# Kernel optimization log

Hardware: AMD Instinct MI355X
Metric: run time of the kernel (lower is better)

Reference implementation:

```python
import jax, jax.numpy as jnp
import numpy as np


def setup_inputs() -> dict:
    key = jax.random.key(0)
    ks = jax.random.split(key, 6)
    B, S, AD, QD, A = 64, 2048, 1024, 1024, 1024
    scale = 0.02
    return {
        "input": jax.random.normal(ks[0], (B, QD), dtype=jnp.float32),
        "context": jax.random.normal(ks[1], (B, S, AD), dtype=jnp.float32),
        "W_pre": jax.random.normal(ks[2], (A, AD), dtype=jnp.float32) * scale,
        "b_pre": jax.random.normal(ks[3], (A,), dtype=jnp.float32) * scale,
        "W_q": jax.random.normal(ks[4], (A, QD), dtype=jnp.float32) * scale,
        "v": jax.random.normal(ks[5], (A,), dtype=jnp.float32) * scale,
    }


def reference(input, context, W_pre, b_pre, W_q, v):
    # precompute = linear_pre(context): [B, S, A]
    precompute = jnp.einsum("bsd,ad->bsa", context, W_pre) + b_pre
    # targetT = linear_q(input): [B, A], broadcast over sourceL
    targetT = jnp.einsum("bq,aq->ba", input, W_q)
    tmp = jnp.tanh(precompute + targetT[:, None, :])  # [B, S, A]
    energy = jnp.einsum("bsa,a->bs", tmp, v)          # linear_v, [B, S]
    score = jax.nn.softmax(energy, axis=1)             # softmax over sourceL
    weightedContext = jnp.einsum("bs,bsd->bd", score, context)
    return weightedContext, score, precompute
```

## Files before the change

### kernel.cpp

```cpp
#include <hip/hip_runtime.h>
#include <hip/hip_bf16.h>

#define BB   64
#define SS   2048
#define MM   (BB*SS)
#define NN   1024
#define KK   1024

typedef short bf16x8s __attribute__((ext_vector_type(8)));
typedef float f32x4   __attribute__((ext_vector_type(4)));

__device__ __forceinline__ short f2bf(float f) {
    union { __hip_bfloat16 h; short s; } u;
    u.h = __float2bfloat16(f);
    return u.s;
}

__device__ __forceinline__ bf16x8s cvt8(float4 a, float4 b) {
    bf16x8s r;
    r[0] = f2bf(a.x); r[1] = f2bf(a.y); r[2] = f2bf(a.z); r[3] = f2bf(a.w);
    r[4] = f2bf(b.x); r[5] = f2bf(b.y); r[6] = f2bf(b.z); r[7] = f2bf(b.w);
    return r;
}

__device__ __forceinline__ float tanh_fast(float x) {
    x = fminf(8.0f, fmaxf(-8.0f, x));
    float e = __expf(2.0f * x);
    return (e - 1.0f) / (e + 1.0f);
}

__device__ __forceinline__ void load_lds16(const void* g, void* l) {
    __builtin_amdgcn_global_load_lds(
        (const __attribute__((address_space(1))) unsigned int*)g,
        (__attribute__((address_space(3))) unsigned int*)l,
        16, 0, 0);
}

__global__ void cvt_bf16_kernel(const float* __restrict__ src,
                                __hip_bfloat16* __restrict__ dst, int n8) {
    int i = blockIdx.x * blockDim.x + threadIdx.x;
    const int stride = gridDim.x * blockDim.x;
    const float4* s4 = (const float4*)src;
    bf16x8s* d8 = (bf16x8s*)dst;
    for (; i < n8; i += stride) {
        d8[i] = cvt8(s4[i * 2], s4[i * 2 + 1]);
    }
}

__global__ void targetT_kernel(const float* __restrict__ input,
                               const float* __restrict__ W_q,
                               float* __restrict__ tgt) {
    __shared__ float inp[KK];
    const int t = threadIdx.x;
    const int b = blockIdx.x;
    const float* inRow = input + (size_t)b * KK;
    for (int i = t; i < KK; i += 256) inp[i] = inRow[i];
    __syncthreads();
    const int w = t >> 6, lane = t & 63;
    const int nbase = blockIdx.y * 256 + w * 64;
    for (int i = 0; i < 64; i++) {
        const int n = nbase + i;
        const float* wq = W_q + (size_t)n * KK;
        float a = 0.f;
        #pragma unroll
        for (int j = 0; j < 16; j++) a += wq[lane + 64 * j] * inp[lane + 64 * j];
        #pragma unroll
        for (int o = 32; o; o >>= 1) a += __shfl_xor(a, o);
        if (lane == 0) tgt[(size_t)b * NN + n] = a;
    }
}

__global__ __launch_bounds__(512, 2) void gemm8_kernel(
    const __hip_bfloat16* __restrict__ ctxb,
    const __hip_bfloat16* __restrict__ wpb,
    const float* __restrict__ bpre,
    const float* __restrict__ tgt,
    const float* __restrict__ vvec,
    float* __restrict__ pre,
    float* __restrict__ energy4,
    int row0)
{
    __shared__ __align__(16) char lds[131072];

    const int nwg  = gridDim.x;
    const int orig = blockIdx.x;
    const int swz  = (orig & 7) * (nwg >> 3) + (orig >> 3);
    const int mTile = swz >> 2;
    const int nTile = swz & 3;
    const int blockM = mTile * 256;
    const int blockN = nTile * 256;

    const int t = threadIdx.x, w = t >> 6, lane = t & 63;
    const int wm = w >> 2, wn = w & 3;
    const int l15 = lane & 15;

    const int r0  = t >> 3;
    const int lc0 = ((t & 7) * 16) ^ ((r0 & 7) << 4);
    const char* aSrc = (const char*)ctxb + (size_t)(blockM + r0) * 2048 + lc0;
    const char* bSrc = (const char*)wpb  + (size_t)(blockN + r0) * 2048 + lc0;

#define STAGE_A(buf, half, T) do { \
    load_lds16(aSrc + (half)*262144 +          (T)*128, &lds[(buf)*32768 + (half)*16384 +        w*1024]); \
    load_lds16(aSrc + (half)*262144 + 131072 + (T)*128, &lds[(buf)*32768 + (half)*16384 + 8192 + w*1024]); \
} while(0)
#define STAGE_B(buf, half, T) do { \
    load_lds16(bSrc + (half)*262144 +          (T)*128, &lds[65536 + (buf)*32768 + (half)*16384 +        w*1024]); \
    load_lds16(bSrc + (half)*262144 + 131072 + (T)*128, &lds[65536 + (buf)*32768 + (half)*16384 + 8192 + w*1024]); \
} while(0)

    const int c16 = (lane >> 4) * 16;
    const int xo  = (lane & 7) << 4;
    const int bk0 = c16 ^ xo;
    const int bk1 = (64 + c16) ^ xo;
    const int aBase = wm * 16384 + l15 * 128;
    const int bBase = 65536 + wn * 8192 + l15 * 128;

    bf16x8s curA[4][2], B0f[2][2], B1f[2][2];

#define READ_A(buf, mbase) do { \
    _Pragma("unroll") \
    for (int mf = 0; mf < 4; mf++) { \
        curA[mf][0] = *(const bf16x8s*)&lds[(buf)*32768 + aBase + ((mbase)+mf)*2048 + bk0]; \
        curA[mf][1] = *(const bf16x8s*)&lds[(buf)*32768 + aBase + ((mbase)+mf)*2048 + bk1]; \
    } } while(0)
#define READ_B(dst, buf, nbase) do { \
    _Pragma("unroll") \
    for (int nf = 0; nf < 2; nf++) { \
        dst[nf][0] = *(const bf16x8s*)&lds[(buf)*32768 + bBase + ((nbase)+nf)*2048 + bk0]; \
        dst[nf][1] = *(const bf16x8s*)&lds[(buf)*32768 + bBase + ((nbase)+nf)*2048 + bk1]; \
    } } while(0)

    f32x4 acc[8][4];
    #pragma unroll
    for (int m = 0; m < 8; m++)
        #pragma unroll
        for (int n = 0; n < 4; n++)
            acc[m][n] = f32x4{0.f, 0.f, 0.f, 0.f};

#define MFMA_Q(mbase, B, nbase) do { \
    __builtin_amdgcn_s_setprio(1); \
    _Pragma("unroll") \
    for (int ks = 0; ks < 2; ks++) \
        _Pragma("unroll") \
        for (int mf = 0; mf < 4; mf++) \
            _Pragma("unroll") \
            for (int nf = 0; nf < 2; nf++) \
                acc[(mbase)+mf][(nbase)+nf] = __builtin_amdgcn_mfma_f32_16x16x32_bf16( \
                    curA[mf][ks], B[nf][ks], acc[(mbase)+mf][(nbase)+nf], 0, 0, 0); \
    __builtin_amdgcn_s_setprio(0); \
} while(0)

#define PH_MID() do { __builtin_amdgcn_sched_barrier(0); \
    __builtin_amdgcn_s_barrier(); \
    asm volatile("s_waitcnt lgkmcnt(0)"); \
    __builtin_amdgcn_sched_barrier(0); } while(0)
#define PH_END() do { __builtin_amdgcn_sched_barrier(0); \
    __builtin_amdgcn_s_barrier(); } while(0)
#define VMCNT(n) do { asm volatile("s_waitcnt vmcnt(" #n ")"); \
    __builtin_amdgcn_sched_barrier(0); } while(0)

    STAGE_A(0, 0, 0); STAGE_A(0, 1, 0);
    STAGE_B(0, 0, 0); STAGE_B(0, 1, 0);
    STAGE_B(1, 0, 1); STAGE_B(1, 1, 1);
    VMCNT(4);
    __builtin_amdgcn_s_barrier();

    #pragma unroll 1
    for (int i = 0; i < 7; i++) {
        const int Tn1 = 2 * i + 1, Tn2 = 2 * i + 2, Tn3 = 2 * i + 3;
        READ_A(0, 0); READ_B(B0f, 0, 0);
        STAGE_A(1, 0, Tn1);
        PH_MID(); MFMA_Q(0, B0f, 0); PH_END();
        READ_B(B1f, 0, 2);
        STAGE_A(1, 1, Tn1);
        PH_MID(); MFMA_Q(0, B1f, 2); PH_END();
        READ_A(0, 4);
        STAGE_B(0, 0, Tn2);
        PH_MID(); MFMA_Q(4, B0f, 0); PH_END();
        STAGE_B(0, 1, Tn2);
        PH_MID(); MFMA_Q(4, B1f, 2);
        VMCNT(4);
        PH_END();
        READ_A(1, 0); READ_B(B0f, 1, 0);
        STAGE_A(0, 0, Tn2);
        PH_MID(); MFMA_Q(0, B0f, 0); PH_END();
        READ_B(B1f, 1, 2);
        STAGE_A(0, 1, Tn2);
        PH_MID(); MFMA_Q(0, B1f, 2); PH_END();
        READ_A(1, 4);
        STAGE_B(1, 0, Tn3);
        PH_MID(); MFMA_Q(4, B0f, 0); PH_END();
        STAGE_B(1, 1, Tn3);
        PH_MID(); MFMA_Q(4, B1f, 2);
        VMCNT(4);
        PH_END();
    }

    READ_A(0, 0); READ_B(B0f, 0, 0);
    STAGE_A(1, 0, 15);
    PH_MID(); MFMA_Q(0, B0f, 0); PH_END();
    READ_B(B1f, 0, 2);
    STAGE_A(1, 1, 15);
    PH_MID(); MFMA_Q(0, B1f, 2); PH_END();
    READ_A(0, 4);
    PH_MID(); MFMA_Q(4, B0f, 0); PH_END();
    PH_MID(); MFMA_Q(4, B1f, 2);
    VMCNT(0);
    PH_END();
    READ_A(1, 0); READ_B(B0f, 1, 0);
    PH_MID(); MFMA_Q(0, B0f, 0); PH_END();
    READ_B(B1f, 1, 2);
    PH_MID(); MFMA_Q(0, B1f, 2); PH_END();
    READ_A(1, 4);
    PH_MID(); MFMA_Q(4, B0f, 0); PH_END();
    PH_MID(); MFMA_Q(4, B1f, 2);

    const int bIdx = (row0 + blockM) >> 11;
    float bp[4], tq[4], vv[4];
    #pragma unroll
    for (int nf = 0; nf < 4; nf++) {
        const int col = blockN + wn * 64 + nf * 16 + l15;
        bp[nf] = bpre[col];
        tq[nf] = tgt[(size_t)bIdx * NN + col];
        vv[nf] = vvec[col];
    }
    const int gr0 = blockM + wm * 128 + ((lane >> 4) << 2);
    const int colBase = blockN + wn * 64 + l15;
    float* epart = energy4 + (size_t)nTile * MM;

    #pragma unroll
    for (int mf = 0; mf < 8; mf++) {
        #pragma unroll
        for (int j = 0; j < 4; j++) {
            const size_t rg = (size_t)row0 + gr0 + mf * 16 + j;
            float* prow = pre + rg * NN + colBase;
            float e = 0.f;
            #pragma unroll
            for (int nf = 0; nf < 4; nf++) {
                const float p = acc[mf][nf][j] + bp[nf];
                prow[nf * 16] = p;
                e += tanh_fast(p + tq[nf]) * vv[nf];
            }
            e += __shfl_xor(e, 1);
            e += __shfl_xor(e, 2);
            e += __shfl_xor(e, 4);
            e += __shfl_xor(e, 8);
            if (l15 == 0) epart[rg] = e;
        }
    }
#undef STAGE_A
#undef STAGE_B
#undef READ_A
#undef READ_B
#undef MFMA_Q
#undef PH_MID
#undef PH_END
#undef VMCNT
}

__global__ __launch_bounds__(256, 2) void gemm_energy_kernel(
    const float* __restrict__ ctx, const float* __restrict__ wpre,
    const float* __restrict__ bpre, const float* __restrict__ tgt,
    const float* __restrict__ vvec, float* __restrict__ pre,
    float* __restrict__ energy4)
{
    __shared__ __align__(16) float As[128 * 32];
    __shared__ __align__(16) float Bs[128 * 32];

    const int orig = blockIdx.x;
    const int swz  = (orig & 7) * 1024 + (orig >> 3);
    const int mTile = swz >> 3;
    const int nTile = swz & 7;
    const size_t blockM = (size_t)mTile * 128;
    const int    blockN = nTile * 128;

    const int t = threadIdx.x, w = t >> 6, lane = t & 63;

    size_t aoff[4], boff[4];
    #pragma unroll
    for (int i = 0; i < 4; i++) {
        const int bb    = i * 4096 + w * 1024 + lane * 16;
        const int row   = bb >> 7;
        const int physc = bb & 127;
        const int logc  = physc ^ ((row & 7) << 4);
        aoff[i] = (blockM + (size_t)row) * (KK * 4) + logc;
        boff[i] = ((size_t)(blockN + row)) * (KK * 4) + logc;
    }
    const char* ctxB  = (const char*)ctx;
    const char* wpreB = (const char*)wpre;

    const int wm = (w >> 1) * 64, wn = (w & 1) * 64;

    int fa0[4], fa1[4], fb0[4], fb1[4];
    const int c0 = (lane >> 4) * 32;
    #pragma unroll
    for (int m = 0; m < 4; m++) {
        const int rA = wm + m * 16 + (lane & 15);
        const int sA = (rA & 7) << 4;
        fa0[m] = rA * 128 + (c0 ^ sA);
        fa1[m] = rA * 128 + ((c0 + 16) ^ sA);
        const int rB = wn + m * 16 + (lane & 15);
        const int sB = (rB & 7) << 4;
        fb0[m] = rB * 128 + (c0 ^ sB);
        fb1[m] = rB * 128 + ((c0 + 16) ^ sB);
    }

    f32x4 acc[4][4];
    #pragma unroll
    for (int m = 0; m < 4; m++)
        #pragma unroll
        for (int n = 0; n < 4; n++)
            acc[m][n] = f32x4{0.f, 0.f, 0.f, 0.f};

    for (int kt = 0; kt < KK / 32; kt++) {
        __syncthreads();
        #pragma unroll
        for (int i = 0; i < 4; i++) {
            load_lds16(ctxB  + aoff[i] + (size_t)kt * 128,
                       (char*)As + i * 4096 + w * 1024);
            load_lds16(wpreB + boff[i] + (size_t)kt * 128,
                       (char*)Bs + i * 4096 + w * 1024);
        }
        __syncthreads();

        bf16x8s af[4], bfr[4];
        #pragma unroll
        for (int m = 0; m < 4; m++) {
            float4 x0 = *(const float4*)((const char*)As + fa0[m]);
            float4 x1 = *(const float4*)((const char*)As + fa1[m]);
            af[m] = cvt8(x0, x1);
            float4 y0 = *(const float4*)((const char*)Bs + fb0[m]);
            float4 y1 = *(const float4*)((const char*)Bs + fb1[m]);
            bfr[m] = cvt8(y0, y1);
        }
        #pragma unroll
        for (int m = 0; m < 4; m++)
            #pragma unroll
            for (int n = 0; n < 4; n++)
                acc[m][n] = __builtin_amdgcn_mfma_f32_16x16x32_bf16(
                    af[m], bfr[n], acc[m][n], 0, 0, 0);
    }

    const int bIdx = (int)(blockM >> 11);
    float bp[4], tq[4], vv[4];
    #pragma unroll
    for (int n = 0; n < 4; n++) {
        const int col = blockN + wn + n * 16 + (lane & 15);
        bp[n] = bpre[col];
        tq[n] = tgt[(size_t)bIdx * NN + col];
        vv[n] = vvec[col];
    }
    const int colBase = blockN + wn + (lane & 15);

    #pragma unroll
    for (int m = 0; m < 4; m++) {
        const size_t rbase = blockM + wm + m * 16 + ((lane >> 4) << 2);
        #pragma unroll
        for (int j = 0; j < 4; j++) {
            const size_t rg = rbase + j;
            float* prow = pre + rg * NN + colBase;
            float e = 0.f;
            #pragma unroll
            for (int n = 0; n < 4; n++) {
                const float p = acc[m][n][j] + bp[n];
                prow[n * 16] = p;
                e += tanh_fast(p + tq[n]) * vv[n];
            }
            e += __shfl_xor(e, 1);
            e += __shfl_xor(e, 2);
            e += __shfl_xor(e, 4);
            e += __shfl_xor(e, 8);
            if ((lane & 15) == 0) atomicAdd(&energy4[rg], e);
        }
    }
}

__global__ void softmax_kernel(const float* __restrict__ energy4,
                               float* __restrict__ score) {
    const int b = blockIdx.x, t = threadIdx.x;
    const int w = t >> 6, lane = t & 63;
    const size_t base = (size_t)b * SS;
    float x[8] = {0.f, 0.f, 0.f, 0.f, 0.f, 0.f, 0.f, 0.f};
    #pragma unroll
    for (int p = 0; p < 4; p++) {
        const float4* e4 = (const float4*)(energy4 + (size_t)p * MM + base);
        float4 v0 = e4[t * 2], v1 = e4[t * 2 + 1];
        x[0] += v0.x; x[1] += v0.y; x[2] += v0.z; x[3] += v0.w;
        x[4] += v1.x; x[5] += v1.y; x[6] += v1.z; x[7] += v1.w;
    }

    float mx = x[0];
    #pragma unroll
    for (int i = 1; i < 8; i++) mx = fmaxf(mx, x[i]);
    #pragma unroll
    for (int o = 32; o; o >>= 1) mx = fmaxf(mx, __shfl_xor(mx, o));
    __shared__ float rmax[4], rsum[4];
    if (lane == 0) rmax[w] = mx;
    __syncthreads();
    mx = fmaxf(fmaxf(rmax[0], rmax[1]), fmaxf(rmax[2], rmax[3]));

    float s = 0.f;
    #pragma unroll
    for (int i = 0; i < 8; i++) { x[i] = __expf(x[i] - mx); s += x[i]; }
    #pragma unroll
    for (int o = 32; o; o >>= 1) s += __shfl_xor(s, o);
    if (lane == 0) rsum[w] = s;
    __syncthreads();
    s = rsum[0] + rsum[1] + rsum[2] + rsum[3];
    const float inv = 1.0f / s;

    float* sc = score + base + t * 8;
    #pragma unroll
    for (int i = 0; i < 8; i++) sc[i] = x[i] * inv;
}

__global__ void wctx_bf16_kernel(const __hip_bfloat16* __restrict__ ctxb,
                                 const float* __restrict__ score,
                                 float* __restrict__ wc) {
    const int b = blockIdx.x, scnk = blockIdx.y, t = threadIdx.x;
    __shared__ float ss[256];
    ss[t] = score[(size_t)b * SS + scnk * 256 + t];
    __syncthreads();
    const ushort4* cr = (const ushort4*)(ctxb + ((size_t)b * SS + (size_t)scnk * 256) * KK) + t;
    float4 a = {0.f, 0.f, 0.f, 0.f};
    #pragma unroll 4
    for (int s = 0; s < 256; s++) {
        const ushort4 c = cr[(size_t)s * 256];
        const float wgt = ss[s];
        a.x += wgt * __uint_as_float((unsigned)c.x << 16);
        a.y += wgt * __uint_as_float((unsigned)c.y << 16);
        a.z += wgt * __uint_as_float((unsigned)c.z << 16);
        a.w += wgt * __uint_as_float((unsigned)c.w << 16);
    }
    float* o = wc + (size_t)b * KK + t * 4;
    atomicAdd(o + 0, a.x);
    atomicAdd(o + 1, a.y);
    atomicAdd(o + 2, a.z);
    atomicAdd(o + 3, a.w);
}

__global__ void wctx_kernel(const float* __restrict__ ctx,
                            const float* __restrict__ score,
                            float* __restrict__ wc) {
    const int b = blockIdx.x, scnk = blockIdx.y, t = threadIdx.x;
    __shared__ float ss[256];
    ss[t] = score[(size_t)b * SS + scnk * 256 + t];
    __syncthreads();
    const float4* cr = (const float4*)(ctx + ((size_t)b * SS + (size_t)scnk * 256) * KK) + t;
    float4 a = {0.f, 0.f, 0.f, 0.f};
    #pragma unroll 4
    for (int s = 0; s < 256; s++) {
        const float4 c = cr[(size_t)s * 256];
        const float wgt = ss[s];
        a.x += wgt * c.x; a.y += wgt * c.y; a.z += wgt * c.z; a.w += wgt * c.w;
    }
    float* o = wc + (size_t)b * KK + t * 4;
    atomicAdd(o + 0, a.x);
    atomicAdd(o + 1, a.y);
    atomicAdd(o + 2, a.z);
    atomicAdd(o + 3, a.w);
}

extern "C" void kernel_launch(void* const* d_in, const int* in_sizes, int n_in,
                              void* d_out, int out_size, void* d_ws, size_t ws_size,
                              hipStream_t stream) {
    const float* input = (const float*)d_in[0];
    const float* ctx   = (const float*)d_in[1];
    const float* W_pre = (const float*)d_in[2];
    const float* b_pre = (const float*)d_in[3];
    const float* W_q   = (const float*)d_in[4];
    const float* v     = (const float*)d_in[5];

    float* out   = (float*)d_out;
    float* wc    = out;
    float* score = out + 65536;
    float* pre   = out + 65536 + 131072;

    float* tgt     = (float*)d_ws;
    float* energy4 = (float*)((char*)d_ws + 262144);
    __hip_bfloat16* wpb  = (__hip_bfloat16*)((char*)d_ws + 262144 + 2097152);
    __hip_bfloat16* ctxb = (__hip_bfloat16*)((char*)d_ws + 262144 + 2097152 + 2097152);

    long long avail = (long long)ws_size - 262144LL - 2097152LL - 2097152LL;
    long long cr = avail > 0 ? (avail / (KK * 2)) : 0;
    cr &= ~511LL;
    int chunk_rows = (int)(cr > MM ? MM : cr);

    hipMemsetAsync(wc, 0, (size_t)BB * KK * sizeof(float), stream);

    targetT_kernel<<<dim3(BB, 4), 256, 0, stream>>>(input, W_q, tgt);

    if (chunk_rows >= 512) {
        cvt_bf16_kernel<<<512, 256, 0, stream>>>(W_pre, wpb, NN * KK / 8);
        for (int r0 = 0; r0 < MM; r0 += chunk_rows) {
            const int rows = (MM - r0) < chunk_rows ? (MM - r0) : chunk_rows;
            const int n8 = rows * KK / 8;
            const int cgrid = (n8 + 255) / 256 > 4096 ? 4096 : (n8 + 255) / 256;
            cvt_bf16_kernel<<<cgrid, 256, 0, stream>>>(
                ctx + (size_t)r0 * KK, ctxb, n8);
            gemm8_kernel<<<dim3((rows / 256) * 4), 512, 0, stream>>>(
                ctxb, wpb, b_pre, tgt, v, pre, energy4, r0);
        }
    } else {
        hipMemsetAsync(energy4, 0, (size_t)4 * MM * sizeof(float), stream);
        gemm_energy_kernel<<<dim3((MM / 128) * (NN / 128)), 256, 0, stream>>>(
            ctx, W_pre, b_pre, tgt, v, pre, energy4);
    }

    softmax_kernel<<<dim3(BB), 256, 0, stream>>>(energy4, score);

    if (chunk_rows >= MM) {
        wctx_bf16_kernel<<<dim3(BB, 8), 256, 0, stream>>>(ctxb, score, wc);
    } else {
        wctx_kernel<<<dim3(BB, 8), 256, 0, stream>>>(ctx, score, wc);
    }
}
```

Before: 620.3 us.

## Halve GEMM pipeline phases per K-tile and use rcp-based tanh

Restructures the bf16 GEMM main loop from eight quarter-phases per double-buffer iteration to four half-phases. Each phase now issues all four B fragments and 32 MFMAs, stages full A/B tiles in one macro, and drops the explicit lgkmcnt(0) waits. This cuts barrier count and gives the scheduler larger MFMA blocks. It also rewrites tanh_fast using a hardware reciprocal instead of a division. The cost is more live B registers and looser control over when LDS reads complete; with the explicit lgkmcnt waits gone, completion of those reads is left to the compiler.

```diff
diff --git a/kernel.cpp b/kernel.cpp
--- a/kernel.cpp
+++ b/kernel.cpp
@@ -26,7 +26,7 @@
 __device__ __forceinline__ float tanh_fast(float x) {
     x = fminf(8.0f, fmaxf(-8.0f, x));
     float e = __expf(2.0f * x);
-    return (e - 1.0f) / (e + 1.0f);
+    return 1.0f - 2.0f * __builtin_amdgcn_rcpf(e + 1.0f);
 }
 
 __device__ __forceinline__ void load_lds16(const void* g, void* l) {
@@ -99,13 +99,17 @@
     const char* aSrc = (const char*)ctxb + (size_t)(blockM + r0) * 2048 + lc0;
     const char* bSrc = (const char*)wpb  + (size_t)(blockN + r0) * 2048 + lc0;
 
-#define STAGE_A(buf, half, T) do { \
-    load_lds16(aSrc + (half)*262144 +          (T)*128, &lds[(buf)*32768 + (half)*16384 +        w*1024]); \
-    load_lds16(aSrc + (half)*262144 + 131072 + (T)*128, &lds[(buf)*32768 + (half)*16384 + 8192 + w*1024]); \
+#define STAGE_AF(buf, T) do { \
+    load_lds16(aSrc +          (T)*128, &lds[(buf)*32768 +         w*1024]); \
+    load_lds16(aSrc + 131072 + (T)*128, &lds[(buf)*32768 +  8192 + w*1024]); \
+    load_lds16(aSrc + 262144 + (T)*128, &lds[(buf)*32768 + 16384 + w*1024]); \
+    load_lds16(aSrc + 393216 + (T)*128, &lds[(buf)*32768 + 24576 + w*1024]); \
 } while(0)
-#define STAGE_B(buf, half, T) do { \
-    load_lds16(bSrc + (half)*262144 +          (T)*128, &lds[65536 + (buf)*32768 + (half)*16384 +        w*1024]); \
-    load_lds16(bSrc + (half)*262144 + 131072 + (T)*128, &lds[65536 + (buf)*32768 + (half)*16384 + 8192 + w*1024]); \
+#define STAGE_BF(buf, T) do { \
+    load_lds16(bSrc +          (T)*128, &lds[65536 + (buf)*32768 +         w*1024]); \
+    load_lds16(bSrc + 131072 + (T)*128, &lds[65536 + (buf)*32768 +  8192 + w*1024]); \
+    load_lds16(bSrc + 262144 + (T)*128, &lds[65536 + (buf)*32768 + 16384 + w*1024]); \
+    load_lds16(bSrc + 393216 + (T)*128, &lds[65536 + (buf)*32768 + 24576 + w*1024]); \
 } while(0)
 
     const int c16 = (lane >> 4) * 16;
@@ -115,7 +119,7 @@
     const int aBase = wm * 16384 + l15 * 128;
     const int bBase = 65536 + wn * 8192 + l15 * 128;
 
-    bf16x8s curA[4][2], B0f[2][2], B1f[2][2];
+    bf16x8s curA[4][2], Bf[4][2];
 
 #define READ_A(buf, mbase) do { \
     _Pragma("unroll") \
@@ -123,11 +127,11 @@
         curA[mf][0] = *(const bf16x8s*)&lds[(buf)*32768 + aBase + ((mbase)+mf)*2048 + bk0]; \
         curA[mf][1] = *(const bf16x8s*)&lds[(buf)*32768 + aBase + ((mbase)+mf)*2048 + bk1]; \
     } } while(0)
-#define READ_B(dst, buf, nbase) do { \
+#define READ_B(buf) do { \
     _Pragma("unroll") \
-    for (int nf = 0; nf < 2; nf++) { \
-        dst[nf][0] = *(const bf16x8s*)&lds[(buf)*32768 + bBase + ((nbase)+nf)*2048 + bk0]; \
-        dst[nf][1] = *(const bf16x8s*)&lds[(buf)*32768 + bBase + ((nbase)+nf)*2048 + bk1]; \
+    for (int nf = 0; nf < 4; nf++) { \
+        Bf[nf][0] = *(const bf16x8s*)&lds[(buf)*32768 + bBase + (nf)*2048 + bk0]; \
+        Bf[nf][1] = *(const bf16x8s*)&lds[(buf)*32768 + bBase + (nf)*2048 + bk1]; \
     } } while(0)
 
     f32x4 acc[8][4];
@@ -137,83 +141,63 @@
         for (int n = 0; n < 4; n++)
             acc[m][n] = f32x4{0.f, 0.f, 0.f, 0.f};
 
-#define MFMA_Q(mbase, B, nbase) do { \
+#define MFMA_H(mbase) do { \
     __builtin_amdgcn_s_setprio(1); \
     _Pragma("unroll") \
     for (int ks = 0; ks < 2; ks++) \
         _Pragma("unroll") \
         for (int mf = 0; mf < 4; mf++) \
             _Pragma("unroll") \
-            for (int nf = 0; nf < 2; nf++) \
-                acc[(mbase)+mf][(nbase)+nf] = __builtin_amdgcn_mfma_f32_16x16x32_bf16( \
-                    curA[mf][ks], B[nf][ks], acc[(mbase)+mf][(nbase)+nf], 0, 0, 0); \
+            for (int nf = 0; nf < 4; nf++) \
+                acc[(mbase)+mf][nf] = __builtin_amdgcn_mfma_f32_16x16x32_bf16( \
+                    curA[mf][ks], Bf[nf][ks], acc[(mbase)+mf][nf], 0, 0, 0); \
     __builtin_amdgcn_s_setprio(0); \
 } while(0)
 
-#define PH_MID() do { __builtin_amdgcn_sched_barrier(0); \
+#define BAR() do { __builtin_amdgcn_sched_barrier(0); \
     __builtin_amdgcn_s_barrier(); \
-    asm volatile("s_waitcnt lgkmcnt(0)"); \
     __builtin_amdgcn_sched_barrier(0); } while(0)
-#define PH_END() do { __builtin_amdgcn_sched_barrier(0); \
-    __builtin_amdgcn_s_barrier(); } while(0)
 #define VMCNT(n) do { asm volatile("s_waitcnt vmcnt(" #n ")"); \
     __builtin_amdgcn_sched_barrier(0); } while(0)
 
-    STAGE_A(0, 0, 0); STAGE_A(0, 1, 0);
-    STAGE_B(0, 0, 0); STAGE_B(0, 1, 0);
-    STAGE_B(1, 0, 1); STAGE_B(1, 1, 1);
+    STAGE_AF(0, 0);
+    STAGE_BF(0, 0);
+    STAGE_BF(1, 1);
     VMCNT(4);
-    __builtin_amdgcn_s_barrier();
+    BAR();
 
     #pragma unroll 1
     for (int i = 0; i < 7; i++) {
-        const int Tn1 = 2 * i + 1, Tn2 = 2 * i + 2, Tn3 = 2 * i + 3;
-        READ_A(0, 0); READ_B(B0f, 0, 0);
-        STAGE_A(1, 0, Tn1);
-        PH_MID(); MFMA_Q(0, B0f, 0); PH_END();
-        READ_B(B1f, 0, 2);
-        STAGE_A(1, 1, Tn1);
-        PH_MID(); MFMA_Q(0, B1f, 2); PH_END();
+        const int To = 2 * i + 1, Te2 = 2 * i + 2, To2 = 2 * i + 3;
+        READ_A(0, 0); READ_B(0);
+        STAGE_AF(1, To);
+        BAR(); MFMA_H(0); BAR();
         READ_A(0, 4);
-        STAGE_B(0, 0, Tn2);
-        PH_MID(); MFMA_Q(4, B0f, 0); PH_END();
-        STAGE_B(0, 1, Tn2);
-        PH_MID(); MFMA_Q(4, B1f, 2);
+        STAGE_BF(0, Te2);
+        BAR(); MFMA_H(4);
         VMCNT(4);
-        PH_END();
-        READ_A(1, 0); READ_B(B0f, 1, 0);
-        STAGE_A(0, 0, Tn2);
-        PH_MID(); MFMA_Q(0, B0f, 0); PH_END();
-        READ_B(B1f, 1, 2);
-        STAGE_A(0, 1, Tn2);
-        PH_MID(); MFMA_Q(0, B1f, 2); PH_END();
+        BAR();
+        READ_A(1, 0); READ_B(1);
+        STAGE_AF(0, Te2);
+        BAR(); MFMA_H(0); BAR();
         READ_A(1, 4);
-        STAGE_B(1, 0, Tn3);
-        PH_MID(); MFMA_Q(4, B0f, 0); PH_END();
-        STAGE_B(1, 1, Tn3);
-        PH_MID(); MFMA_Q(4, B1f, 2);
+        STAGE_BF(1, To2);
+        BAR(); MFMA_H(4);
         VMCNT(4);
-        PH_END();
-    }
-
-    READ_A(0, 0); READ_B(B0f, 0, 0);
-    STAGE_A(1, 0, 15);
-    PH_MID(); MFMA_Q(0, B0f, 0); PH_END();
-    READ_B(B1f, 0, 2);
-    STAGE_A(1, 1, 15);
-    PH_MID(); MFMA_Q(0, B1f, 2); PH_END();
+        BAR();
+    }
+
+    READ_A(0, 0); READ_B(0);
+    STAGE_AF(1, 15);
+    BAR(); MFMA_H(0); BAR();
     READ_A(0, 4);
-    PH_MID(); MFMA_Q(4, B0f, 0); PH_END();
-    PH_MID(); MFMA_Q(4, B1f, 2);
+    BAR(); MFMA_H(4);
     VMCNT(0);
-    PH_END();
-    READ_A(1, 0); READ_B(B0f, 1, 0);
-    PH_MID(); MFMA_Q(0, B0f, 0); PH_END();
-    READ_B(B1f, 1, 2);
-    PH_MID(); MFMA_Q(0, B1f, 2); PH_END();
+    BAR();
+    READ_A(1, 0); READ_B(1);
+    BAR(); MFMA_H(0); BAR();
     READ_A(1, 4);
-    PH_MID(); MFMA_Q(4, B0f, 0); PH_END();
-    PH_MID(); MFMA_Q(4, B1f, 2);
+    BAR(); MFMA_H(4);
 
     const int bIdx = (row0 + blockM) >> 11;
     float bp[4], tq[4], vv[4];
@@ -248,13 +232,12 @@
             if (l15 == 0) epart[rg] = e;
         }
     }
-#undef STAGE_A
-#undef STAGE_B
+#undef STAGE_AF
+#undef STAGE_BF
 #undef READ_A
 #undef READ_B
-#undef MFMA_Q
-#undef PH_MID
-#undef PH_END
+#undef MFMA_H
+#undef BAR
 #undef VMCNT
 }
 
```

Measured after the change: 594.1 us. 4.2% less time.
